# Optimization experiments

Hardware: AMD Instinct MI355X
Metric: run time of the kernel (lower is better)

## Reference

```python
import jax, jax.numpy as jnp
import numpy as np

N = 128      # n_ab: number of independent tiny MLPs
H = 128      # hidden width
L = 4097     # odd alpha grid length, alpha[L//2] == pi/2


def setup_inputs() -> dict:
    key = jax.random.key(0)
    ks = jax.random.split(key, 10)
    alpha = jnp.linspace(0.0, np.pi, L).astype(jnp.float32)
    s = 1.0 / np.sqrt(H)
    w0 = jax.random.normal(ks[0], (N, H, 1), dtype=jnp.float32) * 0.5
    w1 = jax.random.normal(ks[1], (N, H, H), dtype=jnp.float32) * s
    w2 = jax.random.normal(ks[2], (N, H, H), dtype=jnp.float32) * s
    w3 = jax.random.normal(ks[3], (N, 1, H), dtype=jnp.float32) * s
    b0 = jax.random.normal(ks[4], (N, H), dtype=jnp.float32) * 0.1
    b1 = jax.random.normal(ks[5], (N, H), dtype=jnp.float32) * 0.1
    b2 = jax.random.normal(ks[6], (N, H), dtype=jnp.float32) * 0.1
    b3 = jax.random.normal(ks[7], (N, 1), dtype=jnp.float32) * 0.1 + 1.0
    sqrt_a = jax.random.uniform(ks[8], (N,), dtype=jnp.float32, minval=0.5, maxval=1.5)
    return dict(alpha=alpha, w0=w0, w1=w1, w2=w2, w3=w3,
                b0=b0, b1=b1, b2=b2, b3=b3, sqrt_a=sqrt_a)


def _mlp_b(alpha_half, ws, bs):
    # alpha_half: (B,) -> b: (N, B)
    n = ws[0].shape[0]
    x = jnp.broadcast_to(alpha_half[None, :, None], (n, alpha_half.shape[0], 1))
    for w, b in zip(ws[:-1], bs[:-1]):
        x = jax.nn.relu(jnp.einsum('Nij,NBj->NBi', w, x) + b[:, None, :])
    x = jnp.einsum('Nij,NBj->NBi', ws[-1], x) + bs[-1][:, None, :]
    return jnp.square(x)[..., 0]  # (N, B)


def reference(alpha, w0, w1, w2, w3, b0, b1, b2, b3, sqrt_a):
    half = alpha[: alpha.shape[0] // 2 + 1]  # first half incl. pi/2
    ws, bs = (w0, w1, w2, w3), (b0, b1, b2, b3)
    # db/dalpha via jvp with unit tangent: each b[n, j] depends only on
    # alpha_half[j], matching the torch double-autograd trick through z.
    b, db = jax.jvp(lambda a: _mlp_b(a, ws, bs), (half,), (jnp.ones_like(half),))
    b_full = jnp.concatenate([b, b[:, :-1][:, ::-1]], axis=1)          # (N, L)
    db_full = jnp.concatenate([db, -db[:, :-1][:, ::-1]], axis=1)      # (N, L)
    a_full = jnp.square(sqrt_a)[:, None]                               # (N, 1)
    al = alpha[None, :]                                                # (1, L)
    xp = a_full * (jnp.cos(al) - 1.0)
    yp = b_full * jnp.sin(al)
    xp_prime = jnp.broadcast_to(-a_full * jnp.sin(al), b_full.shape)
    yp_prime = b_full * jnp.cos(al) + db_full * jnp.sin(al)
    return xp, yp, xp_prime, yp_prime
```

## Files before the change

### kernel.cpp

```cpp
#include <hip/hip_runtime.h>
#include <math.h>

#define NN 128
#define HH 128
#define LL 4097
#define PH 2049
#define BP 64
#define NTILE 33
#define WS_NEEDED (2u * 128u * 64u * 64u * 16u)

typedef short bf16x8 __attribute__((ext_vector_type(8)));
typedef float f32x4  __attribute__((ext_vector_type(4)));
typedef unsigned int u32;

__device__ __forceinline__ void split1(float x, u32& hi, u32& lo) {
    u32 bx = __float_as_uint(x);
    hi = bx >> 16;
    float hf = __uint_as_float(bx & 0xffff0000u);
    float d  = x - hf;
    lo = (__float_as_uint(d) + 0x8000u) >> 16;
}

__device__ __forceinline__ f32x4 MF(bf16x8 a, bf16x8 b, f32x4 c) {
    return __builtin_amdgcn_mfma_f32_16x16x32_bf16(a, b, c, 0, 0, 0);
}


__global__ __launch_bounds__(512) void presplit(
    const float* __restrict__ w1, const float* __restrict__ w2, uint4* __restrict__ ws)
{
    const int b = blockIdx.x;
    const int m = b >> 7, n = b & 127;
    const float* wn = (m ? w2 : w1) + n * HH * HH;
    uint4* dst = ws + b * 4096;
    const int tid = threadIdx.x;
#pragma unroll
    for (int it = 0; it < 4; ++it) {
        const int s  = tid + it * 512;
        const int l  = s & 63;
        const int fq = s >> 6;
        const int ks = fq & 3, it7 = fq >> 2;
        const int i  = it7 * 16 + (l & 15);
        const int k0 = ks * 32 + (l >> 4) * 8;
        const float4* src = (const float4*)(wn + i * HH + k0);
        const float4 va = src[0], vb = src[1];
        const float v[8] = {va.x, va.y, va.z, va.w, vb.x, vb.y, vb.z, vb.w};
        u32 hd[4], ld_[4];
#pragma unroll
        for (int q = 0; q < 4; ++q) {
            u32 h0, l0, h1, l1;
            split1(v[2*q], h0, l0); split1(v[2*q+1], h1, l1);
            hd[q]  = h0 | (h1 << 16);
            ld_[q] = l0 | (l1 << 16);
        }
        dst[(fq*2 + 0)*64 + l] = make_uint4(hd[0], hd[1], hd[2], hd[3]);
        dst[(fq*2 + 1)*64 + l] = make_uint4(ld_[0], ld_[1], ld_[2], ld_[3]);
    }
}

__device__ __forceinline__ void gemm_regW(const bf16x8* __restrict__ Wf, const char* Xb,
                                          f32x4 acc[4][2], int rw, int cw, int l) {
    const bf16x8* Xf = (const bf16x8*)Xb;
#pragma unroll
    for (int ks = 0; ks < 4; ++ks) {
        bf16x8 Bh[2], Bl[2];
#pragma unroll
        for (int cg = 0; cg < 2; ++cg) {
            const int ct = cw + cg * 4;
            Bh[cg] = Xf[((ct*4 + ks)*2 + 0)*64 + l];
            Bl[cg] = Xf[((ct*4 + ks)*2 + 1)*64 + l];
        }
#pragma unroll
        for (int itl = 0; itl < 4; ++itl) {
            const int IT = rw * 4 + itl;
            const bf16x8 Ah = Wf[((IT*4 + ks)*2 + 0)*64 + l];
            const bf16x8 Al = Wf[((IT*4 + ks)*2 + 1)*64 + l];
#pragma unroll
            for (int cg = 0; cg < 2; ++cg) {
                acc[itl][cg] = MF(Ah, Bh[cg], acc[itl][cg]);
                acc[itl][cg] = MF(Ah, Bl[cg], acc[itl][cg]);
                acc[itl][cg] = MF(Al, Bh[cg], acc[itl][cg]);
            }
        }
    }
}

__global__ __launch_bounds__(512, 4) void sofa_mfma2(
    const float* __restrict__ alpha,
    const float* __restrict__ w0, const float* __restrict__ w3,
    const float* __restrict__ b0, const float* __restrict__ b1,
    const float* __restrict__ b2, const float* __restrict__ b3,
    const float* __restrict__ sqrt_a,
    const uint4* __restrict__ ws,
    float* __restrict__ out)
{
    __shared__ char smem[65536];
    char*  Xb  = smem;
    float* red = (float*)smem;

    const int tile = blockIdx.x, n = blockIdx.y;
    const int tid = threadIdx.x;
    const int l   = tid & 63;
    const int w   = tid >> 6;
    const int rw  = w & 1;
    const int cw  = w >> 1;
    const int t   = l >> 4;

    const bf16x8* W1f = (const bf16x8*)(ws + n * 4096);
    const bf16x8* W2f = (const bf16x8*)(ws + (128 + n) * 4096);

    {
        const float* w0n = w0 + n * HH;
        const float* b0n = b0 + n * HH;
        const int c  = tid & 127;
        const int jb = tid >> 7;
        int p = tile * BP + (c & 63);
        if (p > 2048) p = 2048;
        const float a = alpha[p];
        const bool isdh = c >= 64;
        const int ct = c >> 4;
#pragma unroll
        for (int g8 = 0; g8 < 4; ++g8) {
            u32 hd[4], ld_[4];
#pragma unroll
            for (int q = 0; q < 4; ++q) {
                float vv[2];
#pragma unroll
                for (int e = 0; e < 2; ++e) {
                    const int j = jb * 32 + g8 * 8 + q * 2 + e;
                    const float wv  = w0n[j];
                    const float pre = fmaf(wv, a, b0n[j]);
                    const bool  on  = pre > 0.f;
                    vv[e] = isdh ? (on ? wv : 0.f) : (on ? pre : 0.f);
                }
                u32 h0, l0, h1, l1;
                split1(vv[0], h0, l0); split1(vv[1], h1, l1);
                hd[q]  = h0 | (h1 << 16);
                ld_[q] = l0 | (l1 << 16);
            }
            const int lane = g8 * 16 + (c & 15);
            const int fq   = ct * 4 + jb;
            *(uint4*)(Xb + ((fq*2 + 0)*64 + lane)*16) = make_uint4(hd[0], hd[1], hd[2], hd[3]);
            *(uint4*)(Xb + ((fq*2 + 1)*64 + lane)*16) = make_uint4(ld_[0], ld_[1], ld_[2], ld_[3]);
        }
    }
    __syncthreads();

    f32x4 acc[4][2];
#pragma unroll
    for (int i0 = 0; i0 < 4; ++i0)
#pragma unroll
        for (int c0 = 0; c0 < 2; ++c0) { f32x4 z = {0.f,0.f,0.f,0.f}; acc[i0][c0] = z; }
    gemm_regW(W1f, Xb, acc, rw, cw, l);

    u32 px[4][2][2][2];
    {
        const float* b1n = b1 + n * HH;
#pragma unroll
        for (int itl = 0; itl < 4; ++itl) {
            const int ibase = (rw*4 + itl)*16 + t*4;
            float hv[4], dv[4];
#pragma unroll
            for (int r = 0; r < 4; ++r) {
                const float pre = acc[itl][0][r] + b1n[ibase + r];
                const bool  on  = pre > 0.f;
                hv[r] = on ? pre : 0.f;
                dv[r] = on ? acc[itl][1][r] : 0.f;
            }
#pragma unroll
            for (int cg = 0; cg < 2; ++cg) {
                const float* vs = cg ? dv : hv;
                u32 a0,c0,a1,c1,a2,c2,a3,c3;
                split1(vs[0],a0,c0); split1(vs[1],a1,c1);
                split1(vs[2],a2,c2); split1(vs[3],a3,c3);
                px[itl][cg][0][0] = a0 | (a1 << 16);
                px[itl][cg][0][1] = a2 | (a3 << 16);
                px[itl][cg][1][0] = c0 | (c1 << 16);
                px[itl][cg][1][1] = c2 | (c3 << 16);
            }
        }
    }
    __syncthreads();

    {
#pragma unroll
        for (int itl = 0; itl < 4; ++itl) {
            const int IT   = rw*4 + itl;
            const int lane = ((IT & 1)*2 + (t >> 1))*16 + (l & 15);
            const int off8 = (t & 1)*8;
            const int ksn  = IT >> 1;
#pragma unroll
            for (int cg = 0; cg < 2; ++cg) {
                const int fq = (cw + cg*4)*4 + ksn;
#pragma unroll
                for (int hl = 0; hl < 2; ++hl) {
                    uint2 vv; vv.x = px[itl][cg][hl][0]; vv.y = px[itl][cg][hl][1];
                    *(uint2*)(Xb + ((fq*2 + hl)*64 + lane)*16 + off8) = vv;
                }
            }
        }
    }
    __syncthreads();

    f32x4 acc2[4][2];
#pragma unroll
    for (int i0 = 0; i0 < 4; ++i0)
#pragma unroll
        for (int c0 = 0; c0 < 2; ++c0) { f32x4 z = {0.f,0.f,0.f,0.f}; acc2[i0][c0] = z; }
    gemm_regW(W2f, Xb, acc2, rw, cw, l);

    float sh = 0.f, sd = 0.f;
    {
        const float* b2n = b2 + n * HH;
        const float* w3n = w3 + n * HH;
#pragma unroll
        for (int itl = 0; itl < 4; ++itl) {
            const int ibase = (rw*4 + itl)*16 + t*4;
#pragma unroll
            for (int r = 0; r < 4; ++r) {
                const int   i   = ibase + r;
                const float pre = acc2[itl][0][r] + b2n[i];
                const bool  on  = pre > 0.f;
                const float hv  = on ? pre : 0.f;
                const float dv  = on ? acc2[itl][1][r] : 0.f;
                const float wv  = w3n[i];
                sh = fmaf(wv, hv, sh);
                sd = fmaf(wv, dv, sd);
            }
        }
    }
    sh += __shfl_xor(sh, 16); sh += __shfl_xor(sh, 32);
    sd += __shfl_xor(sd, 16); sd += __shfl_xor(sd, 32);
    __syncthreads();
    if (t == 0) {
        const int p = cw * 16 + (l & 15);
        red[rw * 64 + p]        = sh;
        red[128 + rw * 64 + p]  = sd;
    }
    __syncthreads();

    if (tid < 64) {
        const float oo = b3[n] + red[tid] + red[64 + tid];
        const float d2 = red[128 + tid] + red[192 + tid];
        const float bb = oo * oo;
        const float db = 2.f * oo * d2;
        const float sa = sqrt_a[n];
        const float af = sa * sa;
        const int   NL = NN * LL;
        const int   k1 = tile * BP + tid;
        if (k1 < PH) {
            {
                const float al = alpha[k1];
                const float sn = sinf(al), cs = cosf(al);
                const int base = n * LL + k1;
                out[base]          = af * (cs - 1.f);
                out[NL + base]     = bb * sn;
                out[2 * NL + base] = -af * sn;
                out[3 * NL + base] = fmaf(bb, cs, db * sn);
            }
            if (k1 <= PH - 2) {
                const int   k2  = (LL - 1) - k1;
                const float al2 = alpha[k2];
                const float sn2 = sinf(al2), cs2 = cosf(al2);
                const int base2 = n * LL + k2;
                out[base2]          = af * (cs2 - 1.f);
                out[NL + base2]     = bb * sn2;
                out[2 * NL + base2] = -af * sn2;
                out[3 * NL + base2] = fmaf(bb, cs2, -db * sn2);
            }
        }
    }
}


__device__ __forceinline__ void stageW_fb(const float* __restrict__ wn, char* Wb, int tid) {
#pragma unroll
    for (int it = 0; it < 4; ++it) {
        const int s  = tid + it * 512;
        const int l  = s & 63;
        const int fq = s >> 6;
        const int ks = fq & 3, it7 = fq >> 2;
        const int i  = it7 * 16 + (l & 15);
        const int k0 = ks * 32 + (l >> 4) * 8;
        const float4* src = (const float4*)(wn + i * HH + k0);
        const float4 va = src[0], vb = src[1];
        const float v[8] = {va.x, va.y, va.z, va.w, vb.x, vb.y, vb.z, vb.w};
        u32 hd[4], ld_[4];
#pragma unroll
        for (int q = 0; q < 4; ++q) {
            u32 h0, l0, h1, l1;
            split1(v[2*q], h0, l0); split1(v[2*q+1], h1, l1);
            hd[q]  = h0 | (h1 << 16);
            ld_[q] = l0 | (l1 << 16);
        }
        *(uint4*)(Wb + (((fq*2)+0)*64 + l)*16) = make_uint4(hd[0], hd[1], hd[2], hd[3]);
        *(uint4*)(Wb + (((fq*2)+1)*64 + l)*16) = make_uint4(ld_[0], ld_[1], ld_[2], ld_[3]);
    }
}

__device__ __forceinline__ void gemm128_fb(const char* Wb, const char* Xb,
                                           f32x4 acc[4][2], int rw, int cw, int l) {
    const bf16x8* Wf = (const bf16x8*)Wb;
    const bf16x8* Xf = (const bf16x8*)Xb;
#pragma unroll
    for (int ks = 0; ks < 4; ++ks) {
        bf16x8 Bh[2], Bl[2];
#pragma unroll
        for (int cg = 0; cg < 2; ++cg) {
            const int ct = cw + cg * 4;
            Bh[cg] = Xf[((ct*4 + ks)*2 + 0)*64 + l];
            Bl[cg] = Xf[((ct*4 + ks)*2 + 1)*64 + l];
        }
#pragma unroll
        for (int itl = 0; itl < 4; ++itl) {
            const int IT = rw * 4 + itl;
            const bf16x8 Ah = Wf[((IT*4 + ks)*2 + 0)*64 + l];
            const bf16x8 Al = Wf[((IT*4 + ks)*2 + 1)*64 + l];
#pragma unroll
            for (int cg = 0; cg < 2; ++cg) {
                acc[itl][cg] = MF(Ah, Bh[cg], acc[itl][cg]);
                acc[itl][cg] = MF(Ah, Bl[cg], acc[itl][cg]);
                acc[itl][cg] = MF(Al, Bh[cg], acc[itl][cg]);
            }
        }
    }
}

__global__ __launch_bounds__(512, 2) void sofa_mfma_fb(
    const float* __restrict__ alpha,
    const float* __restrict__ w0, const float* __restrict__ w1,
    const float* __restrict__ w2, const float* __restrict__ w3,
    const float* __restrict__ b0, const float* __restrict__ b1,
    const float* __restrict__ b2, const float* __restrict__ b3,
    const float* __restrict__ sqrt_a,
    float* __restrict__ out)
{
    __shared__ char smem[131072];
    char* Wb = smem;
    char* Xb = smem + 65536;
    float* red = (float*)smem;

    const int tile = blockIdx.x, n = blockIdx.y;
    const int tid = threadIdx.x;
    const int l   = tid & 63;
    const int w   = tid >> 6;
    const int rw  = w & 1;
    const int cw  = w >> 1;
    const int t   = l >> 4;

    stageW_fb(w1 + n * HH * HH, Wb, tid);
    {
        const float* w0n = w0 + n * HH;
        const float* b0n = b0 + n * HH;
        const int c  = tid & 127;
        const int jb = tid >> 7;
        int p = tile * BP + (c & 63);
        if (p > 2048) p = 2048;
        const float a = alpha[p];
        const bool isdh = c >= 64;
        const int ct = c >> 4;
#pragma unroll
        for (int g8 = 0; g8 < 4; ++g8) {
            u32 hd[4], ld_[4];
#pragma unroll
            for (int q = 0; q < 4; ++q) {
                float vv[2];
#pragma unroll
                for (int e = 0; e < 2; ++e) {
                    const int j = jb * 32 + g8 * 8 + q * 2 + e;
                    const float wv  = w0n[j];
                    const float pre = fmaf(wv, a, b0n[j]);
                    const bool  on  = pre > 0.f;
                    vv[e] = isdh ? (on ? wv : 0.f) : (on ? pre : 0.f);
                }
                u32 h0, l0, h1, l1;
                split1(vv[0], h0, l0); split1(vv[1], h1, l1);
                hd[q]  = h0 | (h1 << 16);
                ld_[q] = l0 | (l1 << 16);
            }
            const int lane = g8 * 16 + (c & 15);
            const int fq   = ct * 4 + jb;
            *(uint4*)(Xb + ((fq*2 + 0)*64 + lane)*16) = make_uint4(hd[0], hd[1], hd[2], hd[3]);
            *(uint4*)(Xb + ((fq*2 + 1)*64 + lane)*16) = make_uint4(ld_[0], ld_[1], ld_[2], ld_[3]);
        }
    }
    __syncthreads();

    f32x4 acc[4][2];
#pragma unroll
    for (int i0 = 0; i0 < 4; ++i0)
#pragma unroll
        for (int c0 = 0; c0 < 2; ++c0) { f32x4 z = {0.f,0.f,0.f,0.f}; acc[i0][c0] = z; }
    gemm128_fb(Wb, Xb, acc, rw, cw, l);

    u32 px[4][2][2][2];
    {
        const float* b1n = b1 + n * HH;
#pragma unroll
        for (int itl = 0; itl < 4; ++itl) {
            const int ibase = (rw*4 + itl)*16 + t*4;
            float hv[4], dv[4];
#pragma unroll
            for (int r = 0; r < 4; ++r) {
                const float pre = acc[itl][0][r] + b1n[ibase + r];
                const bool  on  = pre > 0.f;
                hv[r] = on ? pre : 0.f;
                dv[r] = on ? acc[itl][1][r] : 0.f;
            }
#pragma unroll
            for (int cg = 0; cg < 2; ++cg) {
                const float* vs = cg ? dv : hv;
                u32 a0,c0,a1,c1,a2,c2,a3,c3;
                split1(vs[0],a0,c0); split1(vs[1],a1,c1);
                split1(vs[2],a2,c2); split1(vs[3],a3,c3);
                px[itl][cg][0][0] = a0 | (a1 << 16);
                px[itl][cg][0][1] = a2 | (a3 << 16);
                px[itl][cg][1][0] = c0 | (c1 << 16);
                px[itl][cg][1][1] = c2 | (c3 << 16);
            }
        }
    }
    __syncthreads();

    stageW_fb(w2 + n * HH * HH, Wb, tid);
    {
#pragma unroll
        for (int itl = 0; itl < 4; ++itl) {
            const int IT   = rw*4 + itl;
            const int lane = ((IT & 1)*2 + (t >> 1))*16 + (l & 15);
            const int off8 = (t & 1)*8;
            const int ksn  = IT >> 1;
#pragma unroll
            for (int cg = 0; cg < 2; ++cg) {
                const int fq = (cw + cg*4)*4 + ksn;
#pragma unroll
                for (int hl = 0; hl < 2; ++hl) {
                    uint2 vv; vv.x = px[itl][cg][hl][0]; vv.y = px[itl][cg][hl][1];
                    *(uint2*)(Xb + ((fq*2 + hl)*64 + lane)*16 + off8) = vv;
                }
            }
        }
    }
    __syncthreads();

    f32x4 acc2[4][2];
#pragma unroll
    for (int i0 = 0; i0 < 4; ++i0)
#pragma unroll
        for (int c0 = 0; c0 < 2; ++c0) { f32x4 z = {0.f,0.f,0.f,0.f}; acc2[i0][c0] = z; }
    gemm128_fb(Wb, Xb, acc2, rw, cw, l);

    float sh = 0.f, sd = 0.f;
    {
        const float* b2n = b2 + n * HH;
        const float* w3n = w3 + n * HH;
#pragma unroll
        for (int itl = 0; itl < 4; ++itl) {
            const int ibase = (rw*4 + itl)*16 + t*4;
#pragma unroll
            for (int r = 0; r < 4; ++r) {
                const int   i   = ibase + r;
                const float pre = acc2[itl][0][r] + b2n[i];
                const bool  on  = pre > 0.f;
                const float hv  = on ? pre : 0.f;
                const float dv  = on ? acc2[itl][1][r] : 0.f;
                const float wv  = w3n[i];
                sh = fmaf(wv, hv, sh);
                sd = fmaf(wv, dv, sd);
            }
        }
    }
    sh += __shfl_xor(sh, 16); sh += __shfl_xor(sh, 32);
    sd += __shfl_xor(sd, 16); sd += __shfl_xor(sd, 32);
    __syncthreads();
    if (t == 0) {
        const int p = cw * 16 + (l & 15);
        red[rw * 64 + p]        = sh;
        red[128 + rw * 64 + p]  = sd;
    }
    __syncthreads();

    if (tid < 64) {
        const float oo = b3[n] + red[tid] + red[64 + tid];
        const float d2 = red[128 + tid] + red[192 + tid];
        const float bb = oo * oo;
        const float db = 2.f * oo * d2;
        const float sa = sqrt_a[n];
        const float af = sa * sa;
        const int   NL = NN * LL;
        const int   k1 = tile * BP + tid;
        if (k1 < PH) {
            {
                const float al = alpha[k1];
                const float sn = sinf(al), cs = cosf(al);
                const int base = n * LL + k1;
                out[base]          = af * (cs - 1.f);
                out[NL + base]     = bb * sn;
                out[2 * NL + base] = -af * sn;
                out[3 * NL + base] = fmaf(bb, cs, db * sn);
            }
            if (k1 <= PH - 2) {
                const int   k2  = (LL - 1) - k1;
                const float al2 = alpha[k2];
                const float sn2 = sinf(al2), cs2 = cosf(al2);
                const int base2 = n * LL + k2;
                out[base2]          = af * (cs2 - 1.f);
                out[NL + base2]     = bb * sn2;
                out[2 * NL + base2] = -af * sn2;
                out[3 * NL + base2] = fmaf(bb, cs2, -db * sn2);
            }
        }
    }
}

extern "C" void kernel_launch(void* const* d_in, const int* in_sizes, int n_in,
                              void* d_out, int out_size, void* d_ws, size_t ws_size,
                              hipStream_t stream) {
    const float* alpha  = (const float*)d_in[0];
    const float* w0     = (const float*)d_in[1];
    const float* w1     = (const float*)d_in[2];
    const float* w2     = (const float*)d_in[3];
    const float* w3     = (const float*)d_in[4];
    const float* b0     = (const float*)d_in[5];
    const float* b1     = (const float*)d_in[6];
    const float* b2     = (const float*)d_in[7];
    const float* b3     = (const float*)d_in[8];
    const float* sqrt_a = (const float*)d_in[9];
    (void)in_sizes; (void)n_in; (void)out_size;

    dim3 grid(NTILE, NN);
    if (ws_size >= (size_t)WS_NEEDED) {
        uint4* ws = (uint4*)d_ws;
        presplit<<<256, 512, 0, stream>>>(w1, w2, ws);
        sofa_mfma2<<<grid, 512, 0, stream>>>(alpha, w0, w3, b0, b1, b2, b3,
                                             sqrt_a, ws, (float*)d_out);
    } else {
        sofa_mfma_fb<<<grid, 512, 0, stream>>>(alpha, w0, w1, w2, w3,
                                               b0, b1, b2, b3, sqrt_a,
                                               (float*)d_out);
    }
}
```

Before: 215.5 us.

## Halve per-block column tile to 32 with 256-thread blocks and more residency

The main MFMA kernel now handles 32 alpha points per block with 256 threads (4 waves) instead of 64 points with 512 threads. It uses 32KB of LDS and a launch bound of 5 blocks, with twice as many blocks in the grid. This is meant to raise occupancy and shorten each block's critical path. Smaller changes ride along: float4 loads of w0/b0, readfirstlane for wave indices, s_setprio around the GEMMs, and fast __sinf/__cosf with mirror values taken from the symmetry of sin and cos. The cost is that each block now reloads the full pre-split W1/W2 fragments for only half as many columns, doubling weight traffic from global/L2, and the fast trig and symmetry tricks may cost some accuracy.

```diff
diff --git a/kernel.cpp b/kernel.cpp
--- a/kernel.cpp
+++ b/kernel.cpp
@@ -5,6 +5,8 @@
 #define HH 128
 #define LL 4097
 #define PH 2049
+#define BP2 32
+#define NT2 65
 #define BP 64
 #define NTILE 33
 #define WS_NEEDED (2u * 128u * 64u * 64u * 16u)
@@ -66,7 +68,7 @@
         bf16x8 Bh[2], Bl[2];
 #pragma unroll
         for (int cg = 0; cg < 2; ++cg) {
-            const int ct = cw + cg * 4;
+            const int ct = cw + cg * 2;
             Bh[cg] = Xf[((ct*4 + ks)*2 + 0)*64 + l];
             Bl[cg] = Xf[((ct*4 + ks)*2 + 1)*64 + l];
         }
@@ -85,7 +87,7 @@
     }
 }
 
-__global__ __launch_bounds__(512, 4) void sofa_mfma2(
+__global__ __launch_bounds__(256, 5) void sofa_mfma3(
     const float* __restrict__ alpha,
     const float* __restrict__ w0, const float* __restrict__ w3,
     const float* __restrict__ b0, const float* __restrict__ b1,
@@ -94,8 +96,254 @@
     const uint4* __restrict__ ws,
     float* __restrict__ out)
 {
-    __shared__ char smem[65536];
+    __shared__ char smem[32768];
     char*  Xb  = smem;
+    float* red = (float*)smem;
+
+    const int tile = blockIdx.x, n = blockIdx.y;
+    const int tid = threadIdx.x;
+    const int l   = tid & 63;
+    const int w   = tid >> 6;
+    const int rw  = __builtin_amdgcn_readfirstlane(w & 1);
+    const int cw  = __builtin_amdgcn_readfirstlane(w >> 1);
+    const int t   = l >> 4;
+
+    const bf16x8* W1f = (const bf16x8*)(ws + n * 4096);
+    const bf16x8* W2f = (const bf16x8*)(ws + (128 + n) * 4096);
+
+    {
+        const float* w0n = w0 + n * HH;
+        const float* b0n = b0 + n * HH;
+        const int c  = tid & 63;
+        const int jb = tid >> 6;
+        int p = tile * BP2 + (c & 31);
+        if (p > 2048) p = 2048;
+        const float a = alpha[p];
+        const bool isdh = c >= 32;
+        const int ct = c >> 4;
+#pragma unroll
+        for (int g8 = 0; g8 < 4; ++g8) {
+            const float4 wv4a = *(const float4*)(w0n + jb*32 + g8*8);
+            const float4 wv4b = *(const float4*)(w0n + jb*32 + g8*8 + 4);
+            const float4 bv4a = *(const float4*)(b0n + jb*32 + g8*8);
+            const float4 bv4b = *(const float4*)(b0n + jb*32 + g8*8 + 4);
+            const float wvv[8] = {wv4a.x,wv4a.y,wv4a.z,wv4a.w,wv4b.x,wv4b.y,wv4b.z,wv4b.w};
+            const float bvv[8] = {bv4a.x,bv4a.y,bv4a.z,bv4a.w,bv4b.x,bv4b.y,bv4b.z,bv4b.w};
+            u32 hd[4], ld_[4];
+#pragma unroll
+            for (int q = 0; q < 4; ++q) {
+                float vv[2];
+#pragma unroll
+                for (int e = 0; e < 2; ++e) {
+                    const float wv  = wvv[q*2 + e];
+                    const float pre = fmaf(wv, a, bvv[q*2 + e]);
+                    const bool  on  = pre > 0.f;
+                    vv[e] = isdh ? (on ? wv : 0.f) : (on ? pre : 0.f);
+                }
+                u32 h0, l0, h1, l1;
+                split1(vv[0], h0, l0); split1(vv[1], h1, l1);
+                hd[q]  = h0 | (h1 << 16);
+                ld_[q] = l0 | (l1 << 16);
+            }
+            const int lane = g8 * 16 + (c & 15);
+            const int fq   = ct * 4 + jb;
+            *(uint4*)(Xb + ((fq*2 + 0)*64 + lane)*16) = make_uint4(hd[0], hd[1], hd[2], hd[3]);
+            *(uint4*)(Xb + ((fq*2 + 1)*64 + lane)*16) = make_uint4(ld_[0], ld_[1], ld_[2], ld_[3]);
+        }
+    }
+    __syncthreads();
+
+    f32x4 acc[4][2];
+#pragma unroll
+    for (int i0 = 0; i0 < 4; ++i0)
+#pragma unroll
+        for (int c0 = 0; c0 < 2; ++c0) { f32x4 z = {0.f,0.f,0.f,0.f}; acc[i0][c0] = z; }
+    __builtin_amdgcn_s_setprio(1);
+    gemm_regW(W1f, Xb, acc, rw, cw, l);
+    __builtin_amdgcn_s_setprio(0);
+
+    u32 px[4][2][2][2];
+    {
+        const float* b1n = b1 + n * HH;
+#pragma unroll
+        for (int itl = 0; itl < 4; ++itl) {
+            const int ibase = (rw*4 + itl)*16 + t*4;
+            float hv[4], dv[4];
+#pragma unroll
+            for (int r = 0; r < 4; ++r) {
+                const float pre = acc[itl][0][r] + b1n[ibase + r];
+                const bool  on  = pre > 0.f;
+                hv[r] = on ? pre : 0.f;
+                dv[r] = on ? acc[itl][1][r] : 0.f;
+            }
+#pragma unroll
+            for (int cg = 0; cg < 2; ++cg) {
+                const float* vs = cg ? dv : hv;
+                u32 a0,c0,a1,c1,a2,c2,a3,c3;
+                split1(vs[0],a0,c0); split1(vs[1],a1,c1);
+                split1(vs[2],a2,c2); split1(vs[3],a3,c3);
+                px[itl][cg][0][0] = a0 | (a1 << 16);
+                px[itl][cg][0][1] = a2 | (a3 << 16);
+                px[itl][cg][1][0] = c0 | (c1 << 16);
+                px[itl][cg][1][1] = c2 | (c3 << 16);
+            }
+        }
+    }
+    __syncthreads();
+
+    {
+#pragma unroll
+        for (int itl = 0; itl < 4; ++itl) {
+            const int IT   = rw*4 + itl;
+            const int lane = ((IT & 1)*2 + (t >> 1))*16 + (l & 15);
+            const int off8 = (t & 1)*8;
+            const int ksn  = IT >> 1;
+#pragma unroll
+            for (int cg = 0; cg < 2; ++cg) {
+                const int fq = (cw + cg*2)*4 + ksn;
+#pragma unroll
+                for (int hl = 0; hl < 2; ++hl) {
+                    uint2 vv; vv.x = px[itl][cg][hl][0]; vv.y = px[itl][cg][hl][1];
+                    *(uint2*)(Xb + ((fq*2 + hl)*64 + lane)*16 + off8) = vv;
+                }
+            }
+        }
+    }
+    __syncthreads();
+
+    f32x4 acc2[4][2];
+#pragma unroll
+    for (int i0 = 0; i0 < 4; ++i0)
+#pragma unroll
+        for (int c0 = 0; c0 < 2; ++c0) { f32x4 z = {0.f,0.f,0.f,0.f}; acc2[i0][c0] = z; }
+    __builtin_amdgcn_s_setprio(1);
+    gemm_regW(W2f, Xb, acc2, rw, cw, l);
+    __builtin_amdgcn_s_setprio(0);
+
+    float sh = 0.f, sd = 0.f;
+    {
+        const float* b2n = b2 + n * HH;
+        const float* w3n = w3 + n * HH;
+#pragma unroll
+        for (int itl = 0; itl < 4; ++itl) {
+            const int ibase = (rw*4 + itl)*16 + t*4;
+#pragma unroll
+            for (int r = 0; r < 4; ++r) {
+                const int   i   = ibase + r;
+                const float pre = acc2[itl][0][r] + b2n[i];
+                const bool  on  = pre > 0.f;
+                const float hv  = on ? pre : 0.f;
+                const float dv  = on ? acc2[itl][1][r] : 0.f;
+                const float wv  = w3n[i];
+                sh = fmaf(wv, hv, sh);
+                sd = fmaf(wv, dv, sd);
+            }
+        }
+    }
+    sh += __shfl_xor(sh, 16); sh += __shfl_xor(sh, 32);
+    sd += __shfl_xor(sd, 16); sd += __shfl_xor(sd, 32);
+    __syncthreads();
+    if (t == 0) {
+        const int col = cw * 16 + (l & 15);
+        red[rw * 32 + col]       = sh;
+        red[64 + rw * 32 + col]  = sd;
+    }
+    __syncthreads();
+
+    if (tid < 32) {
+        const float oo = b3[n] + red[tid] + red[32 + tid];
+        const float d2 = red[64 + tid] + red[96 + tid];
+        const float bb = oo * oo;
+        const float db = 2.f * oo * d2;
+        const float sa = sqrt_a[n];
+        const float af = sa * sa;
+        const int   NL = NN * LL;
+        const int   k1 = tile * BP2 + tid;
+        if (k1 < PH) {
+            const float al = alpha[k1];
+            const float sn = __sinf(al), cs = __cosf(al);
+            const int base = n * LL + k1;
+            out[base]          = af * (cs - 1.f);
+            out[NL + base]     = bb * sn;
+            out[2 * NL + base] = -af * sn;
+            out[3 * NL + base] = fmaf(bb, cs, db * sn);
+            if (k1 <= PH - 2) {
+                const int base2 = n * LL + (LL - 1) - k1;
+                out[base2]          = af * (-cs - 1.f);
+                out[NL + base2]     = bb * sn;
+                out[2 * NL + base2] = -af * sn;
+                out[3 * NL + base2] = fmaf(bb, -cs, -db * sn);
+            }
+        }
+    }
+}
+
+
+__device__ __forceinline__ void stageW_fb(const float* __restrict__ wn, char* Wb, int tid) {
+#pragma unroll
+    for (int it = 0; it < 4; ++it) {
+        const int s  = tid + it * 512;
+        const int l  = s & 63;
+        const int fq = s >> 6;
+        const int ks = fq & 3, it7 = fq >> 2;
+        const int i  = it7 * 16 + (l & 15);
+        const int k0 = ks * 32 + (l >> 4) * 8;
+        const float4* src = (const float4*)(wn + i * HH + k0);
+        const float4 va = src[0], vb = src[1];
+        const float v[8] = {va.x, va.y, va.z, va.w, vb.x, vb.y, vb.z, vb.w};
+        u32 hd[4], ld_[4];
+#pragma unroll
+        for (int q = 0; q < 4; ++q) {
+            u32 h0, l0, h1, l1;
+            split1(v[2*q], h0, l0); split1(v[2*q+1], h1, l1);
+            hd[q]  = h0 | (h1 << 16);
+            ld_[q] = l0 | (l1 << 16);
+        }
+        *(uint4*)(Wb + (((fq*2)+0)*64 + l)*16) = make_uint4(hd[0], hd[1], hd[2], hd[3]);
+        *(uint4*)(Wb + (((fq*2)+1)*64 + l)*16) = make_uint4(ld_[0], ld_[1], ld_[2], ld_[3]);
+    }
+}
+
+__device__ __forceinline__ void gemm128_fb(const char* Wb, const char* Xb,
+                                           f32x4 acc[4][2], int rw, int cw, int l) {
+    const bf16x8* Wf = (const bf16x8*)Wb;
+    const bf16x8* Xf = (const bf16x8*)Xb;
+#pragma unroll
+    for (int ks = 0; ks < 4; ++ks) {
+        bf16x8 Bh[2], Bl[2];
+#pragma unroll
+        for (int cg = 0; cg < 2; ++cg) {
+            const int ct = cw + cg * 4;
+            Bh[cg] = Xf[((ct*4 + ks)*2 + 0)*64 + l];
+            Bl[cg] = Xf[((ct*4 + ks)*2 + 1)*64 + l];
+        }
+#pragma unroll
+        for (int itl = 0; itl < 4; ++itl) {
+            const int IT = rw * 4 + itl;
+            const bf16x8 Ah = Wf[((IT*4 + ks)*2 + 0)*64 + l];
+            const bf16x8 Al = Wf[((IT*4 + ks)*2 + 1)*64 + l];
+#pragma unroll
+            for (int cg = 0; cg < 2; ++cg) {
+                acc[itl][cg] = MF(Ah, Bh[cg], acc[itl][cg]);
+                acc[itl][cg] = MF(Ah, Bl[cg], acc[itl][cg]);
+                acc[itl][cg] = MF(Al, Bh[cg], acc[itl][cg]);
+            }
+        }
+    }
+}
+
+__global__ __launch_bounds__(512, 2) void sofa_mfma_fb(
+    const float* __restrict__ alpha,
+    const float* __restrict__ w0, const float* __restrict__ w1,
+    const float* __restrict__ w2, const float* __restrict__ w3,
+    const float* __restrict__ b0, const float* __restrict__ b1,
+    const float* __restrict__ b2, const float* __restrict__ b3,
+    const float* __restrict__ sqrt_a,
+    float* __restrict__ out)
+{
+    __shared__ char smem[131072];
+    char* Wb = smem;
+    char* Xb = smem + 65536;
     float* red = (float*)smem;
 
     const int tile = blockIdx.x, n = blockIdx.y;
@@ -106,9 +354,7 @@
     const int cw  = w >> 1;
     const int t   = l >> 4;
 
-    const bf16x8* W1f = (const bf16x8*)(ws + n * 4096);
-    const bf16x8* W2f = (const bf16x8*)(ws + (128 + n) * 4096);
-
+    stageW_fb(w1 + n * HH * HH, Wb, tid);
     {
         const float* w0n = w0 + n * HH;
         const float* b0n = b0 + n * HH;
@@ -151,7 +397,7 @@
     for (int i0 = 0; i0 < 4; ++i0)
 #pragma unroll
         for (int c0 = 0; c0 < 2; ++c0) { f32x4 z = {0.f,0.f,0.f,0.f}; acc[i0][c0] = z; }
-    gemm_regW(W1f, Xb, acc, rw, cw, l);
+    gemm128_fb(Wb, Xb, acc, rw, cw, l);
 
     u32 px[4][2][2][2];
     {
@@ -182,6 +428,7 @@
     }
     __syncthreads();
 
+    stageW_fb(w2 + n * HH * HH, Wb, tid);
     {
 #pragma unroll
         for (int itl = 0; itl < 4; ++itl) {
@@ -207,7 +454,7 @@
     for (int i0 = 0; i0 < 4; ++i0)
 #pragma unroll
         for (int c0 = 0; c0 < 2; ++c0) { f32x4 z = {0.f,0.f,0.f,0.f}; acc2[i0][c0] = z; }
-    gemm_regW(W2f, Xb, acc2, rw, cw, l);
+    gemm128_fb(Wb, Xb, acc2, rw, cw, l);
 
     float sh = 0.f, sd = 0.f;
     {
@@ -272,247 +519,6 @@
     }
 }
 
-
-__device__ __forceinline__ void stageW_fb(const float* __restrict__ wn, char* Wb, int tid) {
-#pragma unroll
-    for (int it = 0; it < 4; ++it) {
-        const int s  = tid + it * 512;
-        const int l  = s & 63;
-        const int fq = s >> 6;
-        const int ks = fq & 3, it7 = fq >> 2;
-        const int i  = it7 * 16 + (l & 15);
-        const int k0 = ks * 32 + (l >> 4) * 8;
-        const float4* src = (const float4*)(wn + i * HH + k0);
-        const float4 va = src[0], vb = src[1];
-        const float v[8] = {va.x, va.y, va.z, va.w, vb.x, vb.y, vb.z, vb.w};
-        u32 hd[4], ld_[4];
-#pragma unroll
-        for (int q = 0; q < 4; ++q) {
-            u32 h0, l0, h1, l1;
-            split1(v[2*q], h0, l0); split1(v[2*q+1], h1, l1);
-            hd[q]  = h0 | (h1 << 16);
-            ld_[q] = l0 | (l1 << 16);
-        }
-        *(uint4*)(Wb + (((fq*2)+0)*64 + l)*16) = make_uint4(hd[0], hd[1], hd[2], hd[3]);
-        *(uint4*)(Wb + (((fq*2)+1)*64 + l)*16) = make_uint4(ld_[0], ld_[1], ld_[2], ld_[3]);
-    }
-}
-
-__device__ __forceinline__ void gemm128_fb(const char* Wb, const char* Xb,
-                                           f32x4 acc[4][2], int rw, int cw, int l) {
-    const bf16x8* Wf = (const bf16x8*)Wb;
-    const bf16x8* Xf = (const bf16x8*)Xb;
-#pragma unroll
-    for (int ks = 0; ks < 4; ++ks) {
-        bf16x8 Bh[2], Bl[2];
-#pragma unroll
-        for (int cg = 0; cg < 2; ++cg) {
-            const int ct = cw + cg * 4;
-            Bh[cg] = Xf[((ct*4 + ks)*2 + 0)*64 + l];
-            Bl[cg] = Xf[((ct*4 + ks)*2 + 1)*64 + l];
-        }
-#pragma unroll
-        for (int itl = 0; itl < 4; ++itl) {
-            const int IT = rw * 4 + itl;
-            const bf16x8 Ah = Wf[((IT*4 + ks)*2 + 0)*64 + l];
-            const bf16x8 Al = Wf[((IT*4 + ks)*2 + 1)*64 + l];
-#pragma unroll
-            for (int cg = 0; cg < 2; ++cg) {
-                acc[itl][cg] = MF(Ah, Bh[cg], acc[itl][cg]);
-                acc[itl][cg] = MF(Ah, Bl[cg], acc[itl][cg]);
-                acc[itl][cg] = MF(Al, Bh[cg], acc[itl][cg]);
-            }
-        }
-    }
-}
-
-__global__ __launch_bounds__(512, 2) void sofa_mfma_fb(
-    const float* __restrict__ alpha,
-    const float* __restrict__ w0, const float* __restrict__ w1,
-    const float* __restrict__ w2, const float* __restrict__ w3,
-    const float* __restrict__ b0, const float* __restrict__ b1,
-    const float* __restrict__ b2, const float* __restrict__ b3,
-    const float* __restrict__ sqrt_a,
-    float* __restrict__ out)
-{
-    __shared__ char smem[131072];
-    char* Wb = smem;
-    char* Xb = smem + 65536;
-    float* red = (float*)smem;
-
-    const int tile = blockIdx.x, n = blockIdx.y;
-    const int tid = threadIdx.x;
-    const int l   = tid & 63;
-    const int w   = tid >> 6;
-    const int rw  = w & 1;
-    const int cw  = w >> 1;
-    const int t   = l >> 4;
-
-    stageW_fb(w1 + n * HH * HH, Wb, tid);
-    {
-        const float* w0n = w0 + n * HH;
-        const float* b0n = b0 + n * HH;
-        const int c  = tid & 127;
-        const int jb = tid >> 7;
-        int p = tile * BP + (c & 63);
-        if (p > 2048) p = 2048;
-        const float a = alpha[p];
-        const bool isdh = c >= 64;
-        const int ct = c >> 4;
-#pragma unroll
-        for (int g8 = 0; g8 < 4; ++g8) {
-            u32 hd[4], ld_[4];
-#pragma unroll
-            for (int q = 0; q < 4; ++q) {
-                float vv[2];
-#pragma unroll
-                for (int e = 0; e < 2; ++e) {
-                    const int j = jb * 32 + g8 * 8 + q * 2 + e;
-                    const float wv  = w0n[j];
-                    const float pre = fmaf(wv, a, b0n[j]);
-                    const bool  on  = pre > 0.f;
-                    vv[e] = isdh ? (on ? wv : 0.f) : (on ? pre : 0.f);
-                }
-                u32 h0, l0, h1, l1;
-                split1(vv[0], h0, l0); split1(vv[1], h1, l1);
-                hd[q]  = h0 | (h1 << 16);
-                ld_[q] = l0 | (l1 << 16);
-            }
-            const int lane = g8 * 16 + (c & 15);
-            const int fq   = ct * 4 + jb;
-            *(uint4*)(Xb + ((fq*2 + 0)*64 + lane)*16) = make_uint4(hd[0], hd[1], hd[2], hd[3]);
-            *(uint4*)(Xb + ((fq*2 + 1)*64 + lane)*16) = make_uint4(ld_[0], ld_[1], ld_[2], ld_[3]);
-        }
-    }
-    __syncthreads();
-
-    f32x4 acc[4][2];
-#pragma unroll
-    for (int i0 = 0; i0 < 4; ++i0)
-#pragma unroll
-        for (int c0 = 0; c0 < 2; ++c0) { f32x4 z = {0.f,0.f,0.f,0.f}; acc[i0][c0] = z; }
-    gemm128_fb(Wb, Xb, acc, rw, cw, l);
-
-    u32 px[4][2][2][2];
-    {
-        const float* b1n = b1 + n * HH;
-#pragma unroll
-        for (int itl = 0; itl < 4; ++itl) {
-            const int ibase = (rw*4 + itl)*16 + t*4;
-            float hv[4], dv[4];
-#pragma unroll
-            for (int r = 0; r < 4; ++r) {
-                const float pre = acc[itl][0][r] + b1n[ibase + r];
-                const bool  on  = pre > 0.f;
-                hv[r] = on ? pre : 0.f;
-                dv[r] = on ? acc[itl][1][r] : 0.f;
-            }
-#pragma unroll
-            for (int cg = 0; cg < 2; ++cg) {
-                const float* vs = cg ? dv : hv;
-                u32 a0,c0,a1,c1,a2,c2,a3,c3;
-                split1(vs[0],a0,c0); split1(vs[1],a1,c1);
-                split1(vs[2],a2,c2); split1(vs[3],a3,c3);
-                px[itl][cg][0][0] = a0 | (a1 << 16);
-                px[itl][cg][0][1] = a2 | (a3 << 16);
-                px[itl][cg][1][0] = c0 | (c1 << 16);
-                px[itl][cg][1][1] = c2 | (c3 << 16);
-            }
-        }
-    }
-    __syncthreads();
-
-    stageW_fb(w2 + n * HH * HH, Wb, tid);
-    {
-#pragma unroll
-        for (int itl = 0; itl < 4; ++itl) {
-            const int IT   = rw*4 + itl;
-            const int lane = ((IT & 1)*2 + (t >> 1))*16 + (l & 15);
-            const int off8 = (t & 1)*8;
-            const int ksn  = IT >> 1;
-#pragma unroll
-            for (int cg = 0; cg < 2; ++cg) {
-                const int fq = (cw + cg*4)*4 + ksn;
-#pragma unroll
-                for (int hl = 0; hl < 2; ++hl) {
-                    uint2 vv; vv.x = px[itl][cg][hl][0]; vv.y = px[itl][cg][hl][1];
-                    *(uint2*)(Xb + ((fq*2 + hl)*64 + lane)*16 + off8) = vv;
-                }
-            }
-        }
-    }
-    __syncthreads();
-
-    f32x4 acc2[4][2];
-#pragma unroll
-    for (int i0 = 0; i0 < 4; ++i0)
-#pragma unroll
-        for (int c0 = 0; c0 < 2; ++c0) { f32x4 z = {0.f,0.f,0.f,0.f}; acc2[i0][c0] = z; }
-    gemm128_fb(Wb, Xb, acc2, rw, cw, l);
-
-    float sh = 0.f, sd = 0.f;
-    {
-        const float* b2n = b2 + n * HH;
-        const float* w3n = w3 + n * HH;
-#pragma unroll
-        for (int itl = 0; itl < 4; ++itl) {
-            const int ibase = (rw*4 + itl)*16 + t*4;
-#pragma unroll
-            for (int r = 0; r < 4; ++r) {
-                const int   i   = ibase + r;
-                const float pre = acc2[itl][0][r] + b2n[i];
-                const bool  on  = pre > 0.f;
-                const float hv  = on ? pre : 0.f;
-                const float dv  = on ? acc2[itl][1][r] : 0.f;
-                const float wv  = w3n[i];
-                sh = fmaf(wv, hv, sh);
-                sd = fmaf(wv, dv, sd);
-            }
-        }
-    }
-    sh += __shfl_xor(sh, 16); sh += __shfl_xor(sh, 32);
-    sd += __shfl_xor(sd, 16); sd += __shfl_xor(sd, 32);
-    __syncthreads();
-    if (t == 0) {
-        const int p = cw * 16 + (l & 15);
-        red[rw * 64 + p]        = sh;
-        red[128 + rw * 64 + p]  = sd;
-    }
-    __syncthreads();
-
-    if (tid < 64) {
-        const float oo = b3[n] + red[tid] + red[64 + tid];
-        const float d2 = red[128 + tid] + red[192 + tid];
-        const float bb = oo * oo;
-        const float db = 2.f * oo * d2;
-        const float sa = sqrt_a[n];
-        const float af = sa * sa;
-        const int   NL = NN * LL;
-        const int   k1 = tile * BP + tid;
-        if (k1 < PH) {
-            {
-                const float al = alpha[k1];
-                const float sn = sinf(al), cs = cosf(al);
-                const int base = n * LL + k1;
-                out[base]          = af * (cs - 1.f);
-                out[NL + base]     = bb * sn;
-                out[2 * NL + base] = -af * sn;
-                out[3 * NL + base] = fmaf(bb, cs, db * sn);
-            }
-            if (k1 <= PH - 2) {
-                const int   k2  = (LL - 1) - k1;
-                const float al2 = alpha[k2];
-                const float sn2 = sinf(al2), cs2 = cosf(al2);
-                const int base2 = n * LL + k2;
-                out[base2]          = af * (cs2 - 1.f);
-                out[NL + base2]     = bb * sn2;
-                out[2 * NL + base2] = -af * sn2;
-                out[3 * NL + base2] = fmaf(bb, cs2, -db * sn2);
-            }
-        }
-    }
-}
-
 extern "C" void kernel_launch(void* const* d_in, const int* in_sizes, int n_in,
                               void* d_out, int out_size, void* d_ws, size_t ws_size,
                               hipStream_t stream) {
@@ -528,13 +534,14 @@
     const float* sqrt_a = (const float*)d_in[9];
     (void)in_sizes; (void)n_in; (void)out_size;
 
-    dim3 grid(NTILE, NN);
     if (ws_size >= (size_t)WS_NEEDED) {
         uint4* ws = (uint4*)d_ws;
         presplit<<<256, 512, 0, stream>>>(w1, w2, ws);
-        sofa_mfma2<<<grid, 512, 0, stream>>>(alpha, w0, w3, b0, b1, b2, b3,
+        dim3 grid(NT2, NN);
+        sofa_mfma3<<<grid, 256, 0, stream>>>(alpha, w0, w3, b0, b1, b2, b3,
                                              sqrt_a, ws, (float*)d_out);
     } else {
+        dim3 grid(NTILE, NN);
         sofa_mfma_fb<<<grid, 512, 0, stream>>>(alpha, w0, w1, w2, w3,
                                                b0, b1, b2, b3, sqrt_a,
                                                (float*)d_out);
```

After: 219.6 us. About the same (+1.9%).
